# Performance work log

Hardware: AMD Instinct MI355X
Metric: run time of the kernel (lower is better)

## Reference

```python
import jax, jax.numpy as jnp
import numpy as np

B, THETA_DIM, Y_DIM, OUT_DIM, WIDTH, NUM_BLOCKS, MULT = 16384, 64, 16, 256, 1024, 4, 2
EPS = 1e-5


def setup_inputs() -> dict:
    key = jax.random.key(0)
    ks = jax.random.split(key, 16)
    hid = MULT * WIDTH
    in_dim = THETA_DIM + 1 + Y_DIM
    inp = {
        "theta_n": jax.random.normal(ks[0], (B, THETA_DIM), jnp.float32),
        "lambda_n": jax.random.normal(ks[1], (B, 1), jnp.float32),
        "y_oh": jax.random.uniform(ks[2], (B, Y_DIM), jnp.float32),
        # input layer
        "W_in": jax.random.normal(ks[3], (in_dim, WIDTH), jnp.float32) * 0.02,
        "b_in": jnp.zeros((WIDTH,), jnp.float32),
        # stacked ResBlockLN params [num_blocks, ...]
        "ln_g": jnp.ones((NUM_BLOCKS, WIDTH), jnp.float32),
        "ln_b": jnp.zeros((NUM_BLOCKS, WIDTH), jnp.float32),
        "w1": jax.random.normal(ks[4], (NUM_BLOCKS, WIDTH, hid), jnp.float32) * 0.02,
        "b1": jnp.zeros((NUM_BLOCKS, hid), jnp.float32),
        "w2": jax.random.normal(ks[5], (NUM_BLOCKS, hid, WIDTH), jnp.float32) * 0.02,
        "b2": jnp.zeros((NUM_BLOCKS, WIDTH), jnp.float32),
        "res_scale": jnp.full((NUM_BLOCKS,), 0.1, jnp.float32),
        # per-class heads stacked [y_dim, width, out_dim]
        "Wh": jax.random.normal(ks[6], (Y_DIM, WIDTH, OUT_DIM), jnp.float32) * 0.02,
        "bh": jnp.zeros((Y_DIM, OUT_DIM), jnp.float32),
    }
    return inp


def _layernorm(x, g, b):
    mu = jnp.mean(x, axis=-1, keepdims=True)
    var = jnp.mean(jnp.square(x - mu), axis=-1, keepdims=True)
    return (x - mu) * jax.lax.rsqrt(var + EPS) * g + b


def reference(theta_n, lambda_n, y_oh, W_in, b_in, ln_g, ln_b, w1, b1, w2, b2, res_scale, Wh, bh):
    x = jnp.concatenate([theta_n, lambda_n, y_oh], axis=1)  # [B, theta+1+y]
    h = jax.nn.gelu(x @ W_in + b_in, approximate=False)      # [B, width]
    for i in range(NUM_BLOCKS):
        z = _layernorm(h, ln_g[i], ln_b[i])
        z = jax.nn.silu(z @ w1[i] + b1[i])
        z = z @ w2[i] + b2[i]
        h = h + res_scale[i] * z
    y_int = jnp.argmax(y_oh, axis=1)                         # [B]
    # compute all heads, then per-sample gather (argmax-routed head)
    all_out = jnp.einsum("bd,kdo->bko", h, Wh) + bh          # [B, y_dim, out_dim]
    out = jnp.take_along_axis(all_out, y_int[:, None, None], axis=1)[:, 0, :]
    return out
```

## Files before the change

### kernel.cpp

```cpp
#include <hip/hip_runtime.h>
#include <hip/hip_bf16.h>
#include <cstdint>
#include <cstddef>

#define B_ROWS 16384
#define WIDTH  1024
#define HID    2048
#define NBLK   4
#define YDIM   16
#define OUTD   256
#define KIN    128
#define MAXM_PER_CLASS 4096

typedef __attribute__((ext_vector_type(8))) short short8;
typedef __attribute__((ext_vector_type(4))) float f32x4;

#define FENCE() asm volatile("" ::: "memory")
#define BAR()   do { FENCE(); __builtin_amdgcn_s_barrier(); FENCE(); } while (0)
#define LGKM0() asm volatile("s_waitcnt lgkmcnt(0)" ::: "memory")
#define VM4()   asm volatile("s_waitcnt vmcnt(4)" ::: "memory")
#define VM0()   asm volatile("s_waitcnt vmcnt(0)" ::: "memory")

__device__ __forceinline__ unsigned short f2bf(float f) {
    union { float f; uint32_t u; } v; v.f = f;
    uint32_t u = v.u;
    uint32_t r = (u + 0x7FFFu + ((u >> 16) & 1u)) >> 16;
    return (unsigned short)r;
}

__device__ __forceinline__ void gload_lds16(const void* g, void* l) {
    __builtin_amdgcn_global_load_lds(
        (const __attribute__((address_space(1))) void*)g,
        (__attribute__((address_space(3))) void*)l, 16, 0, 0);
}

__global__ __launch_bounds__(256)
void prep_x_k(const float* __restrict__ theta, const float* __restrict__ lam,
              const float* __restrict__ yoh, unsigned short* __restrict__ xb)
{
    int tid = threadIdx.x;
    int row = blockIdx.x * 2 + (tid >> 7);
    int j = tid & 127;
    float v;
    if (j < 64)       v = theta[(size_t)row * 64 + j];
    else if (j == 64) v = lam[row];
    else if (j < 81)  v = yoh[(size_t)row * 16 + (j - 65)];
    else              v = 0.f;
    xb[(size_t)row * KIN + j] = f2bf(v);
}

__global__ __launch_bounds__(256)
void bucket_k(const float* __restrict__ yoh, int* __restrict__ counts,
              int* __restrict__ bucket)
{
    __shared__ int cnt_lds[16];
    __shared__ int base_lds[16];
    int tid = threadIdx.x;
    if (tid < 16) cnt_lds[tid] = 0;
    __syncthreads();
    int row = blockIdx.x * 256 + tid;
    const float4* yr = (const float4*)(yoh + (size_t)row * 16);
    int best = 0; float bv = -3.0e38f;
    #pragma unroll
    for (int p = 0; p < 4; ++p) {
        float4 v = yr[p];
        if (v.x > bv) { bv = v.x; best = p * 4 + 0; }
        if (v.y > bv) { bv = v.y; best = p * 4 + 1; }
        if (v.z > bv) { bv = v.z; best = p * 4 + 2; }
        if (v.w > bv) { bv = v.w; best = p * 4 + 3; }
    }
    int mypos = atomicAdd(&cnt_lds[best], 1);
    __syncthreads();
    if (tid < 16) base_lds[tid] = atomicAdd(&counts[tid * 32], cnt_lds[tid]);
    __syncthreads();
    int pos = base_lds[best] + mypos;
    if (pos < MAXM_PER_CLASS) bucket[best * MAXM_PER_CLASS + pos] = row;
}

__global__ __launch_bounds__(256)
void tcvt_k(const float* __restrict__ src, unsigned short* __restrict__ dst,
            int R, int C, int RP)
{
    int b = blockIdx.z;
    src += (size_t)b * R * C;
    dst += (size_t)b * C * RP;
    __shared__ float tile[32][33];
    int tx = threadIdx.x & 31, ty = threadIdx.x >> 5;
    int c0 = blockIdx.x * 32, r0 = blockIdx.y * 32;
    #pragma unroll
    for (int p = 0; p < 4; ++p) {
        int r = r0 + p * 8 + ty;
        float v = (r < R) ? src[(size_t)r * C + c0 + tx] : 0.f;
        tile[p * 8 + ty][tx] = v;
    }
    __syncthreads();
    #pragma unroll
    for (int p = 0; p < 4; ++p) {
        int c = c0 + p * 8 + ty;
        dst[(size_t)c * RP + r0 + tx] = f2bf(tile[tx][p * 8 + ty]);
    }
}

__global__ __launch_bounds__(256)
void ln_k(const float* __restrict__ h, const float* __restrict__ g,
          const float* __restrict__ bb, unsigned short* __restrict__ z)
{
    int row = blockIdx.x;
    int t = threadIdx.x;
    const float4 v = ((const float4*)(h + (size_t)row * WIDTH))[t];
    float s  = v.x + v.y + v.z + v.w;
    float s2 = v.x * v.x + v.y * v.y + v.z * v.z + v.w * v.w;
    #pragma unroll
    for (int off = 32; off > 0; off >>= 1) {
        s  += __shfl_down(s, off);
        s2 += __shfl_down(s2, off);
    }
    __shared__ float red[8];
    int wv = t >> 6;
    if ((t & 63) == 0) { red[wv] = s; red[4 + wv] = s2; }
    __syncthreads();
    float st = 0.f, s2t = 0.f;
    #pragma unroll
    for (int i = 0; i < 4; ++i) { st += red[i]; s2t += red[4 + i]; }
    float mu  = st * (1.f / 1024.f);
    float var = s2t * (1.f / 1024.f) - mu * mu;
    float rs  = rsqrtf(var + 1e-5f);
    float4 gg  = ((const float4*)g)[t];
    float4 bbv = ((const float4*)bb)[t];
    ushort4 o;
    o.x = f2bf((v.x - mu) * rs * gg.x + bbv.x);
    o.y = f2bf((v.y - mu) * rs * gg.y + bbv.y);
    o.z = f2bf((v.z - mu) * rs * gg.z + bbv.z);
    o.w = f2bf((v.w - mu) * rs * gg.w + bbv.w);
    ((ushort4*)(z + (size_t)row * WIDTH))[t] = o;
}

template<int EPI>
__global__ __launch_bounds__(512, 2)
void gemm256_k(const short* __restrict__ A, const short* __restrict__ BT,
               const float* __restrict__ bias,
               float* __restrict__ Cf, unsigned short* __restrict__ Cb,
               const float* __restrict__ rs_ptr, int rs_idx, int writeHb,
               int N, int K, int ntN)
{
    __shared__ short lsA[2][256 * 64];
    __shared__ short lsB[2][256 * 64];

    int tid = threadIdx.x;
    int w = tid >> 6, lane = tid & 63;

    int nwg = gridDim.x;
    int wg  = blockIdx.x;
    int cpx = nwg >> 3;
    int swz = (wg & 7) * cpx + (wg >> 3);
    int bm = swz / ntN, bn = swz % ntN;

    const int wm = w >> 2, wn = w & 3;
    const int lr8 = lane >> 3;
    const int ls8 = lane & 7;
    const int nkt = K >> 6;
    const int nit = nkt >> 1;

    f32x4 acc[8][4];
    #pragma unroll
    for (int i = 0; i < 8; ++i)
        #pragma unroll
        for (int j = 0; j < 4; ++j) acc[i][j] = (f32x4)(0.f);

    auto STAGE_A = [&](int buf, int h, int kt) {
        #pragma unroll
        for (int c = 0; c < 2; ++c) {
            int r  = h * 128 + c * 64 + w * 8 + lr8;
            int sg = ls8 ^ (r & 7);
            const short* g = A + (size_t)(bm * 256 + r) * K + (size_t)kt * 64 + sg * 8;
            gload_lds16(g, &lsA[buf][(h * 128 + c * 64 + w * 8) * 64]);
        }
    };
    auto STAGE_B = [&](int buf, int h, int kt) {
        #pragma unroll
        for (int c = 0; c < 2; ++c) {
            int r  = h * 128 + c * 64 + w * 8 + lr8;
            int sg = ls8 ^ (r & 7);
            const short* g = BT + (size_t)(bn * 256 + r) * K + (size_t)kt * 64 + sg * 8;
            gload_lds16(g, &lsB[buf][(h * 128 + c * 64 + w * 8) * 64]);
        }
    };

    short8 aL[4][2], aH[4][2], bL[2][2], bH[2][2];

    auto RD_AL = [&](int buf) {
        #pragma unroll
        for (int m = 0; m < 4; ++m)
            #pragma unroll
            for (int ks = 0; ks < 2; ++ks) {
                int r = wm * 128 + m * 16 + (lane & 15);
                int s = ks * 4 + (lane >> 4);
                aL[m][ks] = *(const short8*)&lsA[buf][r * 64 + (s ^ (r & 7)) * 8];
            }
    };
    auto RD_AH = [&](int buf) {
        #pragma unroll
        for (int m = 0; m < 4; ++m)
            #pragma unroll
            for (int ks = 0; ks < 2; ++ks) {
                int r = wm * 128 + 64 + m * 16 + (lane & 15);
                int s = ks * 4 + (lane >> 4);
                aH[m][ks] = *(const short8*)&lsA[buf][r * 64 + (s ^ (r & 7)) * 8];
            }
    };
    auto RD_BL = [&](int buf) {
        #pragma unroll
        for (int n = 0; n < 2; ++n)
            #pragma unroll
            for (int ks = 0; ks < 2; ++ks) {
                int r = wn * 64 + n * 16 + (lane & 15);
                int s = ks * 4 + (lane >> 4);
                bL[n][ks] = *(const short8*)&lsB[buf][r * 64 + (s ^ (r & 7)) * 8];
            }
    };
    auto RD_BH = [&](int buf) {
        #pragma unroll
        for (int n = 0; n < 2; ++n)
            #pragma unroll
            for (int ks = 0; ks < 2; ++ks) {
                int r = wn * 64 + 32 + n * 16 + (lane & 15);
                int s = ks * 4 + (lane >> 4);
                bH[n][ks] = *(const short8*)&lsB[buf][r * 64 + (s ^ (r & 7)) * 8];
            }
    };

    auto MM = [&](short8 (&a)[4][2], short8 (&b)[2][2], int mo, int no) {
        __builtin_amdgcn_s_setprio(1);
        #pragma unroll
        for (int ks = 0; ks < 2; ++ks)
            #pragma unroll
            for (int m = 0; m < 4; ++m)
                #pragma unroll
                for (int n = 0; n < 2; ++n)
                    acc[mo + m][no + n] = __builtin_amdgcn_mfma_f32_16x16x32_bf16(
                        a[m][ks], b[n][ks], acc[mo + m][no + n], 0, 0, 0);
        __builtin_amdgcn_s_setprio(0);
    };

    STAGE_B(0, 0, 0); STAGE_B(0, 1, 0);
    STAGE_A(0, 0, 0); STAGE_A(0, 1, 0);
    STAGE_B(1, 0, 1); STAGE_B(1, 1, 1);
    VM4(); BAR();

    for (int it = 0; it < nit; ++it) {
        int T = it * 2;
        bool nl = (it + 1 < nit);
        RD_AL(0); RD_BL(0);
        STAGE_A(1, 0, T + 1);
        BAR(); LGKM0();
        MM(aL, bL, 0, 0);
        BAR();
        RD_BH(0);
        STAGE_A(1, 1, T + 1);
        BAR(); LGKM0();
        MM(aL, bH, 0, 2);
        BAR();
        RD_AH(0);
        if (nl) STAGE_B(0, 0, T + 2);
        BAR(); LGKM0();
        MM(aH, bL, 4, 0);
        BAR();
        if (nl) STAGE_B(0, 1, T + 2);
        BAR(); LGKM0();
        MM(aH, bH, 4, 2);
        if (nl) { VM4(); } else { VM0(); }
        BAR();
        RD_AL(1); RD_BL(1);
        if (nl) STAGE_A(0, 0, T + 2);
        BAR(); LGKM0();
        MM(aL, bL, 0, 0);
        BAR();
        RD_BH(1);
        if (nl) STAGE_A(0, 1, T + 2);
        BAR(); LGKM0();
        MM(aL, bH, 0, 2);
        BAR();
        RD_AH(1);
        if (nl) STAGE_B(1, 0, T + 3);
        BAR(); LGKM0();
        MM(aH, bL, 4, 0);
        BAR();
        if (nl) STAGE_B(1, 1, T + 3);
        BAR(); LGKM0();
        MM(aH, bH, 4, 2);
        if (nl) { VM4(); }
        BAR();
    }

    float rscale = (EPI == 2) ? rs_ptr[rs_idx] : 0.f;
    #pragma unroll
    for (int m = 0; m < 8; ++m) {
        #pragma unroll
        for (int reg = 0; reg < 4; ++reg) {
            int lr = wm * 128 + m * 16 + (lane >> 4) * 4 + reg;
            #pragma unroll
            for (int n = 0; n < 4; ++n) {
                int lc = wn * 64 + n * 16 + (lane & 15);
                float v = acc[m][n][reg];
                size_t idx = ((size_t)bm * 256 + lr) * (size_t)N + bn * 256 + lc;
                float x = v + bias[bn * 256 + lc];
                if (EPI == 1) {
                    Cb[idx] = f2bf(x / (1.f + __expf(-x)));
                } else {
                    float hv = Cf[idx] + rscale * x;
                    Cf[idx] = hv;
                    if (writeHb) Cb[idx] = f2bf(hv);
                }
            }
        }
    }
}

template<int EPI>
__global__ __launch_bounds__(256)
void gemm_k(const short* __restrict__ A, const short* __restrict__ BT,
            const float* __restrict__ bias,
            float* __restrict__ Cf,
            const int* __restrict__ counts, const int* __restrict__ bucket,
            float* __restrict__ outp,
            int N, int K, int ntN)
{
    __shared__ short lsA[2][128 * 64];
    __shared__ short lsB[2][128 * 64];
    __shared__ int rowsLds[128];

    int tid = threadIdx.x;
    int w = tid >> 6, lane = tid & 63;

    int bm = 0, bn = 0, m0 = 0, cnt = 0;
    if (EPI == 3) {
        int cls = blockIdx.z;
        cnt = counts[cls * 32];
        if (cnt > MAXM_PER_CLASS) cnt = MAXM_PER_CLASS;
        m0 = blockIdx.y * 128;
        if (m0 >= cnt) return;
        bn = blockIdx.x;
        if (tid < 128) rowsLds[tid] = bucket[cls * MAXM_PER_CLASS + m0 + tid];
        __syncthreads();
        BT   += (size_t)cls * OUTD * WIDTH;
        bias += cls * OUTD;
    } else {
        int nwg = gridDim.x;
        int wg  = blockIdx.x;
        int cpx = nwg >> 3;
        int swz = (wg & 7) * cpx + (wg >> 3);
        bm = swz / ntN; bn = swz % ntN;
    }

    const int sr = lane >> 3;
    const int ss = lane & 7;
    const int wm = w >> 1, wn = w & 1;
    const int nkt = K >> 6;

    f32x4 acc[4][4];
    #pragma unroll
    for (int i = 0; i < 4; ++i)
        #pragma unroll
        for (int j = 0; j < 4; ++j) acc[i][j] = (f32x4)(0.f);

    auto STAGE = [&](int buf, int kt) {
        #pragma unroll
        for (int c = 0; c < 4; ++c) {
            int r  = w * 32 + c * 8 + sr;
            int sg = ss ^ (r & 7);
            long grow = (EPI == 3) ? (long)rowsLds[r] : ((long)bm * 128 + r);
            const short* ga = A + (size_t)grow * K + (size_t)kt * 64 + sg * 8;
            gload_lds16(ga, &lsA[buf][(w * 32 + c * 8) * 64]);
        }
        #pragma unroll
        for (int c = 0; c < 4; ++c) {
            int r  = w * 32 + c * 8 + sr;
            int sg = ss ^ (r & 7);
            const short* gb = BT + (size_t)(bn * 128 + r) * K + (size_t)kt * 64 + sg * 8;
            gload_lds16(gb, &lsB[buf][(w * 32 + c * 8) * 64]);
        }
    };

    STAGE(0, 0);
    VM0();
    __builtin_amdgcn_s_barrier();

    int cur = 0;
    for (int kt = 0; kt < nkt; ++kt) {
        if (kt + 1 < nkt) STAGE(cur ^ 1, kt + 1);

        #pragma unroll
        for (int ks = 0; ks < 2; ++ks) {
            short8 af[4], bf[4];
            #pragma unroll
            for (int m = 0; m < 4; ++m) {
                int r = wm * 64 + m * 16 + (lane & 15);
                int s = ks * 4 + (lane >> 4);
                af[m] = *(const short8*)&lsA[cur][r * 64 + (s ^ (r & 7)) * 8];
            }
            #pragma unroll
            for (int n = 0; n < 4; ++n) {
                int r = wn * 64 + n * 16 + (lane & 15);
                int s = ks * 4 + (lane >> 4);
                bf[n] = *(const short8*)&lsB[cur][r * 64 + (s ^ (r & 7)) * 8];
            }
            __builtin_amdgcn_s_setprio(1);
            #pragma unroll
            for (int m = 0; m < 4; ++m)
                #pragma unroll
                for (int n = 0; n < 4; ++n)
                    acc[m][n] = __builtin_amdgcn_mfma_f32_16x16x32_bf16(af[m], bf[n], acc[m][n], 0, 0, 0);
            __builtin_amdgcn_s_setprio(0);
        }

        VM0();
        __builtin_amdgcn_s_barrier();
        cur ^= 1;
    }

    #pragma unroll
    for (int m = 0; m < 4; ++m) {
        #pragma unroll
        for (int reg = 0; reg < 4; ++reg) {
            int lr = wm * 64 + m * 16 + (lane >> 4) * 4 + reg;
            #pragma unroll
            for (int n = 0; n < 4; ++n) {
                int lc = wn * 64 + n * 16 + (lane & 15);
                float v = acc[m][n][reg];
                if (EPI == 0) {
                    size_t idx = ((size_t)bm * 128 + lr) * (size_t)N + bn * 128 + lc;
                    float x = v + bias[bn * 128 + lc];
                    Cf[idx] = 0.5f * x * (1.f + erff(x * 0.70710678118f));
                } else {
                    if (m0 + lr < cnt) {
                        int orow = rowsLds[lr];
                        int oc = bn * 128 + lc;
                        outp[(size_t)orow * OUTD + oc] = v + bias[oc];
                    }
                }
            }
        }
    }
}

extern "C" void kernel_launch(void* const* d_in, const int* in_sizes, int n_in,
                              void* d_out, int out_size, void* d_ws, size_t ws_size,
                              hipStream_t stream)
{
    const float* theta = (const float*)d_in[0];
    const float* lam   = (const float*)d_in[1];
    const float* yoh   = (const float*)d_in[2];
    const float* W_in  = (const float*)d_in[3];
    const float* b_in  = (const float*)d_in[4];
    const float* ln_g  = (const float*)d_in[5];
    const float* ln_b  = (const float*)d_in[6];
    const float* w1    = (const float*)d_in[7];
    const float* b1    = (const float*)d_in[8];
    const float* w2    = (const float*)d_in[9];
    const float* b2    = (const float*)d_in[10];
    const float* rsc   = (const float*)d_in[11];
    const float* Wh    = (const float*)d_in[12];
    const float* bh    = (const float*)d_in[13];
    float* out = (float*)d_out;

    char* p = (char*)d_ws;
    auto alloc = [&](size_t bytes) -> char* {
        char* r = p; p += (bytes + 255) & ~(size_t)255; return r;
    };
    float*          h    = (float*)         alloc((size_t)B_ROWS * WIDTH * 4);
    unsigned short* hb   = (unsigned short*)alloc((size_t)B_ROWS * WIDTH * 2);
    unsigned short* z    = (unsigned short*)alloc((size_t)B_ROWS * WIDTH * 2);
    unsigned short* t    = (unsigned short*)alloc((size_t)B_ROWS * HID * 2);
    unsigned short* xb   = (unsigned short*)alloc((size_t)B_ROWS * KIN * 2);
    unsigned short* w1T  = (unsigned short*)alloc((size_t)NBLK * HID * WIDTH * 2);
    unsigned short* w2T  = (unsigned short*)alloc((size_t)NBLK * WIDTH * HID * 2);
    unsigned short* WhT  = (unsigned short*)alloc((size_t)YDIM * OUTD * WIDTH * 2);
    unsigned short* WiT  = (unsigned short*)alloc((size_t)WIDTH * KIN * 2);
    int*            bucket = (int*)alloc((size_t)YDIM * MAXM_PER_CLASS * 4);
    int*            counts = (int*)alloc(16 * 32 * 4);

    hipMemsetAsync(bucket, 0, (size_t)YDIM * MAXM_PER_CLASS * 4, stream);
    hipMemsetAsync(counts, 0, 16 * 32 * 4, stream);

    prep_x_k<<<B_ROWS / 2, 256, 0, stream>>>(theta, lam, yoh, xb);
    bucket_k<<<B_ROWS / 256, 256, 0, stream>>>(yoh, counts, bucket);

    tcvt_k<<<dim3(WIDTH / 32, KIN / 32, 1),    256, 0, stream>>>(W_in, WiT, 81,   WIDTH, KIN);
    tcvt_k<<<dim3(HID / 32,   WIDTH / 32, 4),  256, 0, stream>>>(w1,   w1T, WIDTH, HID,  WIDTH);
    tcvt_k<<<dim3(WIDTH / 32, HID / 32, 4),    256, 0, stream>>>(w2,   w2T, HID,  WIDTH, HID);
    tcvt_k<<<dim3(OUTD / 32,  WIDTH / 32, 16), 256, 0, stream>>>(Wh,   WhT, WIDTH, OUTD, WIDTH);

    gemm_k<0><<<(B_ROWS / 128) * (WIDTH / 128), 256, 0, stream>>>(
        (const short*)xb, (const short*)WiT, b_in, h,
        nullptr, nullptr, nullptr, WIDTH, KIN, WIDTH / 128);

    for (int i = 0; i < NBLK; ++i) {
        ln_k<<<B_ROWS, 256, 0, stream>>>(h, ln_g + i * WIDTH, ln_b + i * WIDTH, z);
        gemm256_k<1><<<(B_ROWS / 256) * (HID / 256), 512, 0, stream>>>(
            (const short*)z, (const short*)(w1T + (size_t)i * HID * WIDTH), b1 + i * HID,
            nullptr, t, nullptr, 0, 0, HID, WIDTH, HID / 256);
        gemm256_k<2><<<(B_ROWS / 256) * (WIDTH / 256), 512, 0, stream>>>(
            (const short*)t, (const short*)(w2T + (size_t)i * WIDTH * HID), b2 + i * WIDTH,
            h, hb, rsc, i, (i == NBLK - 1) ? 1 : 0, WIDTH, HID, WIDTH / 256);
    }

    gemm_k<3><<<dim3(OUTD / 128, MAXM_PER_CLASS / 128, YDIM), 256, 0, stream>>>(
        (const short*)hb, (const short*)WhT, bh, nullptr,
        counts, bucket, out, OUTD, WIDTH, OUTD / 128);

    (void)in_sizes; (void)n_in; (void)out_size; (void)ws_size; (void)rsc;
}
```

Baseline: 988.7 us.

## Replace LDS-staged 256-tile w2 GEMM with register-direct 128-tile kernel

The second residual GEMM (hidden to width, K=2048) moves from the 256x256 LDS double-buffered kernel to a new 128x128 kernel. The new kernel loads bf16 fragments straight from global memory into registers, double-buffers them, and issues MFMA with no LDS and no barriers. The aim is to raise parallelism, since the N=1024 GEMM had only 256 workgroups at 256-wide tiles, and to remove barrier overhead. The cost is less data reuse: each wave pulls strided global rows without LDS sharing, which could become bandwidth or latency bound.

New measurement: 1.592 ms. 1.61x slower.

```diff
diff --git a/kernel.cpp b/kernel.cpp
--- a/kernel.cpp
+++ b/kernel.cpp
@@ -135,6 +135,86 @@
     ((ushort4*)(z + (size_t)row * WIDTH))[t] = o;
 }
 
+__global__ __launch_bounds__(256, 2)
+void rgemm_k(const short* __restrict__ A, const short* __restrict__ BT,
+             const float* __restrict__ bias,
+             float* __restrict__ Cf, unsigned short* __restrict__ Cb,
+             const float* __restrict__ rs_ptr, int rs_idx, int writeHb,
+             int N, int K, int ntN)
+{
+    int tid = threadIdx.x;
+    int w = tid >> 6, lane = tid & 63;
+
+    int nwg = gridDim.x;
+    int wg  = blockIdx.x;
+    int cpx = nwg >> 3;
+    int swz = (wg & 7) * cpx + (wg >> 3);
+    int bm = swz / ntN, bn = swz % ntN;
+
+    const int wm = w >> 1, wn = w & 1;
+    const int frow  = lane & 15;
+    const int fksl  = (lane >> 4) * 8;
+
+    const short* pa = A  + (size_t)(bm * 128 + wm * 64 + frow) * K + fksl;
+    const short* pb = BT + (size_t)(bn * 128 + wn * 64 + frow) * K + fksl;
+
+    f32x4 acc[4][4];
+    #pragma unroll
+    for (int i = 0; i < 4; ++i)
+        #pragma unroll
+        for (int j = 0; j < 4; ++j) acc[i][j] = (f32x4)(0.f);
+
+    short8 a0[4], b0[4], a1[4], b1[4];
+
+    auto LD = [&](short8 (&av)[4], short8 (&bv)[4], int kk) {
+        const short* pak = pa + (size_t)kk * 32;
+        const short* pbk = pb + (size_t)kk * 32;
+        #pragma unroll
+        for (int m = 0; m < 4; ++m)
+            av[m] = *(const short8*)(pak + (size_t)(m * 16) * K);
+        #pragma unroll
+        for (int n = 0; n < 4; ++n)
+            bv[n] = *(const short8*)(pbk + (size_t)(n * 16) * K);
+    };
+    auto MM = [&](short8 (&av)[4], short8 (&bv)[4]) {
+        __builtin_amdgcn_s_setprio(1);
+        #pragma unroll
+        for (int m = 0; m < 4; ++m)
+            #pragma unroll
+            for (int n = 0; n < 4; ++n)
+                acc[m][n] = __builtin_amdgcn_mfma_f32_16x16x32_bf16(av[m], bv[n], acc[m][n], 0, 0, 0);
+        __builtin_amdgcn_s_setprio(0);
+    };
+
+    const int nks = K >> 5;
+    LD(a0, b0, 0);
+    for (int kk = 0; kk < nks; kk += 2) {
+        if (kk + 1 < nks) LD(a1, b1, kk + 1);
+        MM(a0, b0);
+        if (kk + 2 < nks) LD(a0, b0, kk + 2);
+        if (kk + 1 < nks) MM(a1, b1);
+    }
+
+    float rscale = rs_ptr[rs_idx];
+    #pragma unroll
+    for (int m = 0; m < 4; ++m) {
+        #pragma unroll
+        for (int reg = 0; reg < 4; ++reg) {
+            int lr = wm * 64 + m * 16 + (lane >> 4) * 4 + reg;
+            #pragma unroll
+            for (int n = 0; n < 4; ++n) {
+                int lc = wn * 64 + n * 16 + (lane & 15);
+                float v = acc[m][n][reg];
+                size_t idx = ((size_t)bm * 128 + lr) * (size_t)N + bn * 128 + lc;
+                float x = v + bias[bn * 128 + lc];
+                float hv = Cf[idx] + rscale * x;
+                Cf[idx] = hv;
+                if (writeHb) Cb[idx] = f2bf(hv);
+            }
+        }
+    }
+}
+
 template<int EPI>
 __global__ __launch_bounds__(512, 2)
 void gemm256_k(const short* __restrict__ A, const short* __restrict__ BT,
@@ -292,7 +372,6 @@
         BAR();
     }
 
-    float rscale = (EPI == 2) ? rs_ptr[rs_idx] : 0.f;
     #pragma unroll
     for (int m = 0; m < 8; ++m) {
         #pragma unroll
@@ -304,16 +383,11 @@
                 float v = acc[m][n][reg];
                 size_t idx = ((size_t)bm * 256 + lr) * (size_t)N + bn * 256 + lc;
                 float x = v + bias[bn * 256 + lc];
-                if (EPI == 1) {
-                    Cb[idx] = f2bf(x / (1.f + __expf(-x)));
-                } else {
-                    float hv = Cf[idx] + rscale * x;
-                    Cf[idx] = hv;
-                    if (writeHb) Cb[idx] = f2bf(hv);
-                }
-            }
-        }
-    }
+                Cb[idx] = f2bf(x / (1.f + __expf(-x)));
+            }
+        }
+    }
+    (void)Cf; (void)rs_ptr; (void)rs_idx; (void)writeHb;
 }
 
 template<int EPI>
@@ -499,9 +573,9 @@
         gemm256_k<1><<<(B_ROWS / 256) * (HID / 256), 512, 0, stream>>>(
             (const short*)z, (const short*)(w1T + (size_t)i * HID * WIDTH), b1 + i * HID,
             nullptr, t, nullptr, 0, 0, HID, WIDTH, HID / 256);
-        gemm256_k<2><<<(B_ROWS / 256) * (WIDTH / 256), 512, 0, stream>>>(
+        rgemm_k<<<(B_ROWS / 128) * (WIDTH / 128), 256, 0, stream>>>(
             (const short*)t, (const short*)(w2T + (size_t)i * WIDTH * HID), b2 + i * WIDTH,
-            h, hb, rsc, i, (i == NBLK - 1) ? 1 : 0, WIDTH, HID, WIDTH / 256);
+            h, hb, rsc, i, (i == NBLK - 1) ? 1 : 0, WIDTH, HID, WIDTH / 128);
     }
 
     gemm_k<3><<<dim3(OUTD / 128, MAXM_PER_CLASS / 128, YDIM), 256, 0, stream>>>(
```
